# Performance work log

Measured on AMD Instinct MI355X. Metric: run time of the kernel, lower is better.

Reference implementation:

```python
import jax, jax.numpy as jnp
import numpy as np
import math

# dims
B, S, HID = 1, 4096, 2048
NH = 16            # num_attention_heads
Q_LORA = 768
KV_LORA = 512
D_ROPE = 64        # qk_rope_head_dim
D_V = 128          # v_head_dim
TOP_K = 1024       # dsa_top_k
EPS = 1e-6
ROPE_BASE = 1e7
YARN_SCALE = 32.0


def _rms_norm(x, w, eps=EPS):
    xf = x.astype(jnp.float32)
    var = jnp.mean(xf * xf, axis=-1, keepdims=True)
    return (w * (xf * jax.lax.rsqrt(var + eps))).astype(x.dtype)


def _rotate_half(x):
    h = x.shape[-1] // 2
    return jnp.concatenate([-x[..., h:], x[..., :h]], axis=-1)


def _yarn_cos_sin(seq_len):
    # _yarn_find_correction_dims returns (mid, mid) => entire inv_freq is interpolated (divided by scale)
    inv_freq = 1.0 / (ROPE_BASE ** (jnp.arange(0, D_ROPE, 2, dtype=jnp.float32) / D_ROPE))
    inv_freq = inv_freq / YARN_SCALE
    t = jnp.arange(seq_len, dtype=jnp.float32) / YARN_SCALE
    freqs = t[:, None] * inv_freq[None, :]          # [S, D_ROPE/2]
    emb = jnp.concatenate([freqs, freqs], axis=-1)  # [S, D_ROPE]
    mscale2 = (0.1 * math.log(YARN_SCALE) + 1.0) ** 2  # mscale * mscale_all_dim
    return jnp.cos(emb) * mscale2, jnp.sin(emb) * mscale2


def setup_inputs() -> dict:
    key = jax.random.key(0)
    ks = jax.random.split(key, 10)
    std = 0.02
    return {
        'hidden_states': jax.random.normal(ks[0], (B, S, HID), dtype=jnp.float32),
        'position_ids': jnp.broadcast_to(jnp.arange(S), (B, S)),
        'dsa_indices': jnp.sort(jax.random.randint(ks[1], (B, 1, TOP_K), 0, S), axis=-1),
        'wq_a': jax.random.normal(ks[2], (HID, Q_LORA), dtype=jnp.float32) * std,
        'q_a_ln_w': jnp.ones((Q_LORA,), dtype=jnp.float32),
        'wq_b': jax.random.normal(ks[3], (Q_LORA, NH * D_V), dtype=jnp.float32) * std,
        'wq_rope': jax.random.normal(ks[4], (Q_LORA, NH * D_ROPE), dtype=jnp.float32) * std,
        'wkv_a': jax.random.normal(ks[5], (HID, KV_LORA + D_ROPE), dtype=jnp.float32) * std,
        'kv_a_ln_w': jnp.ones((KV_LORA,), dtype=jnp.float32),
        'wkv_b': jax.random.normal(ks[6], (KV_LORA, NH * 2 * D_V), dtype=jnp.float32) * std,
        'wo': jax.random.normal(ks[7], (NH * D_V, HID), dtype=jnp.float32) * std,
    }


def reference(hidden_states, position_ids, dsa_indices, wq_a, q_a_ln_w, wq_b,
              wq_rope, wkv_a, kv_a_ln_w, wkv_b, wo):
    bsz, seq_len, _ = hidden_states.shape

    # low-rank Q path (MLA)
    q_latent = _rms_norm(hidden_states @ wq_a, q_a_ln_w)            # [B,S,Q_LORA]
    q = (q_latent @ wq_b).reshape(bsz, seq_len, NH, D_V)            # [B,S,H,D_V]
    q_rope = (q_latent @ wq_rope).reshape(bsz, seq_len, NH, D_ROPE)

    # low-rank KV path with MQA rope channel
    kv_lr = hidden_states @ wkv_a                                   # [B,S,KV_LORA+D_ROPE]
    kv_latent = _rms_norm(kv_lr[..., :KV_LORA], kv_a_ln_w)
    k_rope = kv_lr[..., KV_LORA:]                                   # [B,S,D_ROPE]
    k_and_v = (kv_latent @ wkv_b).reshape(bsz, seq_len, NH, 2 * D_V)
    k = k_and_v[..., :D_V]
    v = k_and_v[..., D_V:]
    k_rope = jnp.broadcast_to(k_rope[:, :, None, :], (bsz, seq_len, NH, D_ROPE))

    # YaRN rotary embedding
    cos, sin = _yarn_cos_sin(seq_len)                               # [S,D_ROPE]
    cos_p = cos[position_ids][:, :, None, :]                        # [B,S,1,D_ROPE]
    sin_p = sin[position_ids][:, :, None, :]
    q_rope = q_rope * cos_p + _rotate_half(q_rope) * sin_p
    k_rope = k_rope * cos_p + _rotate_half(k_rope) * sin_p

    q_full = jnp.concatenate([q, q_rope], axis=-1)                  # [B,S,H,D_V+D_ROPE]
    k_full = jnp.concatenate([k, k_rope], axis=-1)

    # DSA: gather top-k KV positions per batch (dsa_indices[b,0,:])
    idx = dsa_indices[:, 0, :]                                      # [B,TOP_K]
    k_g = jnp.take_along_axis(k_full, idx[:, :, None, None], axis=1)  # [B,K,H,D]
    v_g = jnp.take_along_axis(v, idx[:, :, None, None], axis=1)       # [B,K,H,D_V]

    scale = 1.0 / math.sqrt(D_V + D_ROPE)
    scores = jnp.einsum('bqhd,bkhd->bhqk', q_full, k_g) * scale     # [B,H,S,K]
    probs = jax.nn.softmax(scores, axis=-1)
    attn = jnp.einsum('bhqk,bkhd->bqhd', probs, v_g)                # [B,S,H,D_V]
    out = attn.reshape(bsz, seq_len, NH * D_V) @ wo                 # [B,S,HID]
    return out
```

## Files before the change

kernel.cpp:

```cpp
#include <hip/hip_runtime.h>
#include <hip/hip_bf16.h>
#include <math.h>

#define S_LEN 4096
#define HIDDEN 2048
#define NH 16
#define QLORA 768
#define KVLORA 512
#define DROPE 64
#define DV 128
#define TOPK 1024
#define DQK 192

typedef __attribute__((ext_vector_type(4))) float f32x4;
typedef __attribute__((ext_vector_type(8))) __bf16 bf16x8;
typedef unsigned short u16;
typedef unsigned int u32;

__device__ __forceinline__ u16 f2bf(float f) {
    union { float f; u32 u; } v; v.f = f;
    u32 r = v.u + 0x7fffu + ((v.u >> 16) & 1u);
    return (u16)(r >> 16);
}

__device__ __forceinline__ void gll16(const u16* g, u16* l) {
    __builtin_amdgcn_global_load_lds((const void*)g, (void*)l, 16, 0, 0);
}

__global__ __launch_bounds__(256) void k_cast(const float* __restrict__ src,
                                              u16* __restrict__ dst, int n4) {
    int i = blockIdx.x * 256 + threadIdx.x;
    if (i >= n4) return;
    float4 v = ((const float4*)src)[i];
    union { u16 h[4]; uint2 u; } o;
    o.h[0] = f2bf(v.x); o.h[1] = f2bf(v.y);
    o.h[2] = f2bf(v.z); o.h[3] = f2bf(v.w);
    ((uint2*)dst)[i] = o.u;
}

__global__ __launch_bounds__(256) void k_yarn(const int* __restrict__ pos_ids,
                                              float* __restrict__ cos_t,
                                              float* __restrict__ sin_t) {
    int idx = blockIdx.x * 256 + threadIdx.x;
    if (idx >= S_LEN * 32) return;
    int s = idx >> 5, i = idx & 31;
    float pos = (float)pos_ids[s];
    float inv = expf(-(float)i * 0.503690489092448f) * (1.0f / 1024.0f);
    float ang = pos * inv;
    const float MS2 = 1.8132604f;
    float sv, cv;
    sincosf(ang, &sv, &cv);
    cos_t[idx] = cv * MS2;
    sin_t[idx] = sv * MS2;
}

__global__ __launch_bounds__(256) void k_transpose(const float* __restrict__ src,
                                                   u16* __restrict__ dst,
                                                   int K, int N) {
    __shared__ u16 t[32][33];
    int n0 = blockIdx.x * 32, k0 = blockIdx.y * 32;
    int tx = threadIdx.x & 31, ty = threadIdx.x >> 5;
    #pragma unroll
    for (int i = 0; i < 32; i += 8)
        t[ty + i][tx] = f2bf(src[(long)(k0 + ty + i) * N + n0 + tx]);
    __syncthreads();
    #pragma unroll
    for (int i = 0; i < 32; i += 8)
        dst[(long)(n0 + ty + i) * K + k0 + tx] = t[tx][ty + i];
}

template <int MODE>
__global__ __launch_bounds__(256) void k_gemm(const u16* __restrict__ A,
                                              const u16* __restrict__ Bt,
                                              void* __restrict__ out0,
                                              void* __restrict__ out1,
                                              const float* __restrict__ cos_t,
                                              const float* __restrict__ sin_t,
                                              int M, int N, int K) {
    __shared__ u16 lA[128 * 32];
    __shared__ u16 lB[128 * 32];
    const int bm = blockIdx.y, bn = blockIdx.x;
    const int tid = threadIdx.x;
    const int lane = tid & 63, wid = tid >> 6;
    const int wr = wid >> 1, wc = wid & 1;
    const int l15 = lane & 15, l4 = lane >> 4;

    f32x4 acc[4][4];
    #pragma unroll
    for (int i = 0; i < 4; ++i)
        #pragma unroll
        for (int j = 0; j < 4; ++j) acc[i][j] = f32x4{0.f, 0.f, 0.f, 0.f};

    const int srow = wid * 32 + (lane >> 2);
    const int scol = (lane & 3) * 8;
    const u16* gA = A + (long)(bm * 128 + srow) * K + scol;
    const u16* gB = Bt + (long)(bn * 128 + srow) * K + scol;
    u16* lA0 = lA + wid * 1024;
    u16* lB0 = lB + wid * 1024;
    const long kstep16 = 16L * K;

    const int nkt = K >> 5;
    for (int kt = 0; kt < nkt; ++kt) {
        const u16* pa = gA + kt * 32;
        const u16* pb = gB + kt * 32;
        gll16(pa, lA0);
        gll16(pa + kstep16, lA0 + 512);
        gll16(pb, lB0);
        gll16(pb + kstep16, lB0 + 512);
        __syncthreads();

        bf16x8 af[4], bfr[4];
        #pragma unroll
        for (int mr = 0; mr < 4; ++mr)
            af[mr] = *(const bf16x8*)(&lA[(wr * 64 + mr * 16 + l15) * 32 + l4 * 8]);
        #pragma unroll
        for (int nc = 0; nc < 4; ++nc)
            bfr[nc] = *(const bf16x8*)(&lB[(wc * 64 + nc * 16 + l15) * 32 + l4 * 8]);
        #pragma unroll
        for (int mr = 0; mr < 4; ++mr)
            #pragma unroll
            for (int nc = 0; nc < 4; ++nc)
                acc[mr][nc] = __builtin_amdgcn_mfma_f32_16x16x32_bf16(
                    af[mr], bfr[nc], acc[mr][nc], 0, 0, 0);
        __syncthreads();
    }

    const int row0 = bm * 128 + wr * 64;
    const int col0 = bn * 128 + wc * 64;
    #pragma unroll
    for (int mr = 0; mr < 4; ++mr) {
        #pragma unroll
        for (int nc = 0; nc < 4; ++nc) {
            #pragma unroll
            for (int jj = 0; jj < 4; ++jj) {
                int row = row0 + mr * 16 + l4 * 4 + jj;
                int col = col0 + nc * 16 + l15;
                float v = acc[mr][nc][jj];
                if (MODE == 0) {
                    if (col < QLORA)
                        ((float*)out0)[(long)row * QLORA + col] = v;
                    else if (col < QLORA + KVLORA + DROPE)
                        ((float*)out1)[(long)row * (KVLORA + DROPE) + (col - QLORA)] = v;
                } else if (MODE == 1) {
                    if (col < NH * DV) {
                        int h = col >> 7, d = col & 127;
                        ((u16*)out0)[((long)h * S_LEN + row) * DQK + d] = f2bf(v);
                    } else {
                        int c2 = col - NH * DV;
                        int h = c2 >> 6, j = c2 & 63, i = j & 31;
                        float c = cos_t[row * 32 + i], sn = sin_t[row * 32 + i];
                        float xp = acc[mr][nc ^ 2][jj];
                        float val = (j < 32) ? v * c - xp * sn : v * c + xp * sn;
                        ((u16*)out0)[((long)h * S_LEN + row) * DQK + DV + j] = f2bf(val);
                    }
                } else if (MODE == 2) {
                    int h = col >> 8, rr = col & 255;
                    if (rr < 128)
                        ((u16*)out0)[((long)h * S_LEN + row) * DV + rr] = f2bf(v);
                    else
                        ((u16*)out1)[((long)h * S_LEN + row) * DV + (rr - 128)] = f2bf(v);
                } else {
                    ((float*)out0)[(long)row * N + col] = v;
                }
            }
        }
    }
}

__global__ __launch_bounds__(256) void k_rms_q(const float* __restrict__ q_lr,
                                               const float* __restrict__ w,
                                               u16* __restrict__ q_latent) {
    int s = blockIdx.x;
    const float* x = q_lr + (long)s * QLORA;
    int t = threadIdx.x;
    float v0 = x[t], v1 = x[t + 256], v2 = x[t + 512];
    float ss = v0 * v0 + v1 * v1 + v2 * v2;
    #pragma unroll
    for (int off = 32; off >= 1; off >>= 1) ss += __shfl_xor(ss, off);
    __shared__ float red[4];
    if ((t & 63) == 0) red[t >> 6] = ss;
    __syncthreads();
    ss = red[0] + red[1] + red[2] + red[3];
    float inv = rsqrtf(ss / (float)QLORA + 1e-6f);
    u16* o = q_latent + (long)s * QLORA;
    o[t]       = f2bf(v0 * inv * w[t]);
    o[t + 256] = f2bf(v1 * inv * w[t + 256]);
    o[t + 512] = f2bf(v2 * inv * w[t + 512]);
}

__global__ __launch_bounds__(256) void k_kv_norm_rope(const float* __restrict__ kv_lr,
                                                      const float* __restrict__ w,
                                                      const float* __restrict__ cos_t,
                                                      const float* __restrict__ sin_t,
                                                      u16* __restrict__ kv_latent,
                                                      u16* __restrict__ krope) {
    int s = blockIdx.x;
    const float* x = kv_lr + (long)s * (KVLORA + DROPE);
    int t = threadIdx.x;
    float v0 = x[t], v1 = x[t + 256];
    float ss = v0 * v0 + v1 * v1;
    #pragma unroll
    for (int off = 32; off >= 1; off >>= 1) ss += __shfl_xor(ss, off);
    __shared__ float red[4];
    if ((t & 63) == 0) red[t >> 6] = ss;
    __syncthreads();
    ss = red[0] + red[1] + red[2] + red[3];
    float inv = rsqrtf(ss / (float)KVLORA + 1e-6f);
    u16* o = kv_latent + (long)s * KVLORA;
    o[t]       = f2bf(v0 * inv * w[t]);
    o[t + 256] = f2bf(v1 * inv * w[t + 256]);
    if (t < DROPE) {
        int i = t & 31;
        float c = cos_t[s * 32 + i], sn = sin_t[s * 32 + i];
        float xr = x[KVLORA + t];
        float xp = x[KVLORA + ((t < 32) ? t + 32 : t - 32)];
        float val = (t < 32) ? xr * c - xp * sn : xr * c + xp * sn;
        krope[(long)s * DROPE + t] = f2bf(val);
    }
}

__global__ void k_gather(const int* __restrict__ idx,
                         const u16* __restrict__ k_buf,
                         const u16* __restrict__ v_buf,
                         const u16* __restrict__ krope,
                         u16* __restrict__ k_g, u16* __restrict__ v_g_t) {
    int j = blockIdx.x, h = blockIdx.y, t = threadIdx.x;
    int src = idx[j];
    const uint4* kb = (const uint4*)(k_buf + ((long)h * S_LEN + src) * DV);
    const uint4* kr = (const uint4*)(krope + (long)src * DROPE);
    uint4* kgp = (uint4*)(k_g + ((long)h * TOPK + j) * DQK);
    if (t < 16)       kgp[t] = kb[t];
    else if (t < 24)  kgp[t] = kr[t - 16];
    u32 vv = *(const u32*)(v_buf + ((long)h * S_LEN + src) * DV + t * 2);
    int kt = j >> 6, jin = j & 63;
    u16* base = v_g_t + ((long)(h * 16 + kt) * 128) * 64 + jin;
    base[(2 * t) * 64]     = (u16)(vv & 0xffff);
    base[(2 * t + 1) * 64] = (u16)(vv >> 16);
}

__global__ __launch_bounds__(256) void k_attn(const u16* __restrict__ qf,
                                              const u16* __restrict__ kg,
                                              const u16* __restrict__ vgt,
                                              u16* __restrict__ attn_out) {
    __shared__ u16 lK[64 * 200];
    __shared__ u16 lVt[128 * 72];
    __shared__ u16 lP[4][16 * 72];
    const int b = blockIdx.x;
    const int h = (b & 7) * 2 + ((b >> 3) & 1);
    const int qt = b >> 4;
    const int tid = threadIdx.x, lane = tid & 63, wid = tid >> 6;
    const int l15 = lane & 15, l4 = lane >> 4;

    bf16x8 qfr[2][6];
    #pragma unroll
    for (int qs = 0; qs < 2; ++qs) {
        const u16* qrow = qf + ((long)h * S_LEN + qt * 128 + wid * 32 + qs * 16 + l15) * DQK + l4 * 8;
        #pragma unroll
        for (int kd = 0; kd < 6; ++kd) qfr[qs][kd] = *(const bf16x8*)(qrow + kd * 32);
    }
    float m[2][4], l[2][4];
    #pragma unroll
    for (int qs = 0; qs < 2; ++qs)
        #pragma unroll
        for (int jj = 0; jj < 4; ++jj) { m[qs][jj] = -1e30f; l[qs][jj] = 0.f; }
    f32x4 acc_o[2][8];
    #pragma unroll
    for (int qs = 0; qs < 2; ++qs)
        #pragma unroll
        for (int nc = 0; nc < 8; ++nc) acc_o[qs][nc] = f32x4{0.f, 0.f, 0.f, 0.f};

    const int krow = tid >> 2, kseg = (tid & 3) * 48;
    u16* lPw = lP[wid];
    const float scale = 0.07216878364870323f;

    for (int kt = 0; kt < TOPK / 64; ++kt) {
        {
            const u16* src = kg + ((long)h * TOPK + kt * 64 + krow) * DQK + kseg;
            u16* dst = &lK[krow * 200 + kseg];
            #pragma unroll
            for (int u = 0; u < 6; ++u)
                *(uint4*)(dst + u * 8) = *(const uint4*)(src + u * 8);
        }
        {
            const u16* src = vgt + ((long)(h * 16 + kt) * 128) * 64 + tid * 32;
            u16* dst = &lVt[(tid >> 1) * 72 + (tid & 1) * 32];
            #pragma unroll
            for (int c = 0; c < 4; ++c)
                *(uint4*)(dst + c * 8) = *(const uint4*)(src + c * 8);
        }
        __syncthreads();

        #pragma unroll
        for (int qs = 0; qs < 2; ++qs) {
            f32x4 sa[4];
            #pragma unroll
            for (int kc = 0; kc < 4; ++kc) {
                sa[kc] = f32x4{0.f, 0.f, 0.f, 0.f};
                #pragma unroll
                for (int kd = 0; kd < 6; ++kd) {
                    bf16x8 kf = *(const bf16x8*)(&lK[(kc * 16 + l15) * 200 + kd * 32 + l4 * 8]);
                    sa[kc] = __builtin_amdgcn_mfma_f32_16x16x32_bf16(qfr[qs][kd], kf, sa[kc], 0, 0, 0);
                }
                sa[kc] *= scale;
            }
            float fac[4], psum[4];
            #pragma unroll
            for (int jj = 0; jj < 4; ++jj) {
                float mx = fmaxf(fmaxf(sa[0][jj], sa[1][jj]), fmaxf(sa[2][jj], sa[3][jj]));
                #pragma unroll
                for (int off = 1; off <= 8; off <<= 1) mx = fmaxf(mx, __shfl_xor(mx, off));
                float mnew = fmaxf(m[qs][jj], mx);
                fac[jj] = __expf(m[qs][jj] - mnew);
                m[qs][jj] = mnew;
                psum[jj] = 0.f;
            }
            #pragma unroll
            for (int kc = 0; kc < 4; ++kc) {
                #pragma unroll
                for (int jj = 0; jj < 4; ++jj) {
                    float p = __expf(sa[kc][jj] - m[qs][jj]);
                    psum[jj] += p;
                    lPw[(l4 * 4 + jj) * 72 + kc * 16 + l15] = f2bf(p);
                }
            }
            #pragma unroll
            for (int jj = 0; jj < 4; ++jj) {
                #pragma unroll
                for (int off = 1; off <= 8; off <<= 1) psum[jj] += __shfl_xor(psum[jj], off);
                l[qs][jj] = l[qs][jj] * fac[jj] + psum[jj];
            }
            #pragma unroll
            for (int nc = 0; nc < 8; ++nc)
                #pragma unroll
                for (int jj = 0; jj < 4; ++jj) acc_o[qs][nc][jj] *= fac[jj];
            #pragma unroll
            for (int kc2 = 0; kc2 < 2; ++kc2) {
                bf16x8 pf = *(const bf16x8*)(&lPw[l15 * 72 + kc2 * 32 + l4 * 8]);
                #pragma unroll
                for (int nc = 0; nc < 8; ++nc) {
                    bf16x8 vf = *(const bf16x8*)(&lVt[(nc * 16 + l15) * 72 + kc2 * 32 + l4 * 8]);
                    acc_o[qs][nc] = __builtin_amdgcn_mfma_f32_16x16x32_bf16(pf, vf, acc_o[qs][nc], 0, 0, 0);
                }
            }
        }
        __syncthreads();
    }
    #pragma unroll
    for (int qs = 0; qs < 2; ++qs) {
        int row = qt * 128 + wid * 32 + qs * 16 + l4 * 4;
        #pragma unroll
        for (int nc = 0; nc < 8; ++nc)
            #pragma unroll
            for (int jj = 0; jj < 4; ++jj) {
                float v = acc_o[qs][nc][jj] / l[qs][jj];
                attn_out[(long)(row + jj) * (NH * DV) + h * DV + nc * 16 + l15] = f2bf(v);
            }
    }
}

extern "C" void kernel_launch(void* const* d_in, const int* in_sizes, int n_in,
                              void* d_out, int out_size, void* d_ws, size_t ws_size,
                              hipStream_t stream) {
    const float* hs      = (const float*)d_in[0];
    const int*   pos     = (const int*)d_in[1];
    const int*   dsa     = (const int*)d_in[2];
    const float* wq_a    = (const float*)d_in[3];
    const float* q_ln    = (const float*)d_in[4];
    const float* wq_b    = (const float*)d_in[5];
    const float* wq_rope = (const float*)d_in[6];
    const float* wkv_a   = (const float*)d_in[7];
    const float* kv_ln   = (const float*)d_in[8];
    const float* wkv_b   = (const float*)d_in[9];
    const float* wo      = (const float*)d_in[10];
    float* out = (float*)d_out;

    char* ws = (char*)d_ws;
    auto alloc = [&](size_t bytes) {
        char* p = ws; ws += (bytes + 255) & ~(size_t)255; return p;
    };
    u16* W1t  = (u16*)alloc(1408L * 2048 * 2);
    u16* W2t  = (u16*)alloc(3072L * 768 * 2);
    u16* W3t  = (u16*)alloc(4096L * 512 * 2);
    u16* W4t  = (u16*)alloc(2048L * 2048 * 2);
    float* q_lr  = (float*)alloc(4096L * 768 * 4);
    float* kv_lr = (float*)alloc(4096L * 576 * 4);
    u16* q_latent   = (u16*)alloc(4096L * 768 * 2);
    u16* kv_latent  = (u16*)alloc(4096L * 512 * 2);
    u16* q_full     = (u16*)alloc(16L * 4096 * 192 * 2);
    u16* k_buf      = (u16*)alloc(16L * 4096 * 128 * 2);
    u16* v_buf      = (u16*)alloc(16L * 4096 * 128 * 2);
    float* cos_t    = (float*)alloc(4096L * 32 * 4);
    float* sin_t    = (float*)alloc(4096L * 32 * 4);
    char* late = alloc(16L * 4096 * 2 * 2);
    u16* hs_bf = (u16*)late;
    u16* k_g   = (u16*)late;
    u16* v_g_t = k_g + 16L * 1024 * 192;
    u16* krope = v_g_t + 16L * 1024 * 128;
    u16* attn_o = (u16*)q_lr;

    k_yarn<<<dim3(512), dim3(256), 0, stream>>>(pos, cos_t, sin_t);
    k_cast<<<dim3(8192), dim3(256), 0, stream>>>(hs, hs_bf, 4096 * 2048 / 4);

    k_transpose<<<dim3(768 / 32, 2048 / 32), 256, 0, stream>>>(wq_a, W1t, 2048, 768);
    k_transpose<<<dim3(576 / 32, 2048 / 32), 256, 0, stream>>>(wkv_a, W1t + 768L * 2048, 2048, 576);
    k_transpose<<<dim3(2048 / 32, 768 / 32), 256, 0, stream>>>(wq_b, W2t, 768, 2048);
    k_transpose<<<dim3(1024 / 32, 768 / 32), 256, 0, stream>>>(wq_rope, W2t + 2048L * 768, 768, 1024);
    k_transpose<<<dim3(4096 / 32, 512 / 32), 256, 0, stream>>>(wkv_b, W3t, 512, 4096);
    k_transpose<<<dim3(2048 / 32, 2048 / 32), 256, 0, stream>>>(wo, W4t, 2048, 2048);

    k_gemm<0><<<dim3(11, 32), 256, 0, stream>>>(hs_bf, W1t, q_lr, kv_lr, nullptr, nullptr, 4096, 1408, 2048);
    k_rms_q<<<4096, 256, 0, stream>>>(q_lr, q_ln, q_latent);
    k_kv_norm_rope<<<4096, 256, 0, stream>>>(kv_lr, kv_ln, cos_t, sin_t, kv_latent, krope);
    k_gemm<1><<<dim3(24, 32), 256, 0, stream>>>(q_latent, W2t, q_full, nullptr, cos_t, sin_t, 4096, 3072, 768);
    k_gemm<2><<<dim3(32, 32), 256, 0, stream>>>(kv_latent, W3t, k_buf, v_buf, nullptr, nullptr, 4096, 4096, 512);
    k_gather<<<dim3(1024, 16), 64, 0, stream>>>(dsa, k_buf, v_buf, krope, k_g, v_g_t);
    k_attn<<<dim3(512), 256, 0, stream>>>(q_full, k_g, v_g_t, attn_o);
    k_gemm<3><<<dim3(16, 32), 256, 0, stream>>>(attn_o, W4t, out, nullptr, nullptr, nullptr, 4096, 2048, 2048);
}
```

Baseline: 502.4 us.

## Load K and V fragments directly from global memory, drop LDS staging and barriers

The attention kernel no longer stages K and V tiles into shared memory with block-wide barriers. Each wave now loads its MFMA fragments straight from global memory and reuses each K/V fragment across both 16-row query sub-tiles. A per-subtile P buffer lets the PV MFMAs for both sub-tiles be interleaved. This removes the LDS round trip and the __syncthreads stalls and raises occupancy through lower LDS use. In exchange, all 4 waves re-read the same K/V from global/L2 with strided 16-byte accesses.

After: 554.7 us. +10.4%, slower.

```diff
diff --git a/kernel.cpp b/kernel.cpp
--- a/kernel.cpp
+++ b/kernel.cpp
@@ -242,9 +242,7 @@
                                               const u16* __restrict__ kg,
                                               const u16* __restrict__ vgt,
                                               u16* __restrict__ attn_out) {
-    __shared__ u16 lK[64 * 200];
-    __shared__ u16 lVt[128 * 72];
-    __shared__ u16 lP[4][16 * 72];
+    __shared__ u16 lP[4][2][16 * 72];
     const int b = blockIdx.x;
     const int h = (b & 7) * 2 + ((b >> 3) & 1);
     const int qt = b >> 4;
@@ -269,44 +267,33 @@
         #pragma unroll
         for (int nc = 0; nc < 8; ++nc) acc_o[qs][nc] = f32x4{0.f, 0.f, 0.f, 0.f};
 
-    const int krow = tid >> 2, kseg = (tid & 3) * 48;
-    u16* lPw = lP[wid];
     const float scale = 0.07216878364870323f;
 
     for (int kt = 0; kt < TOPK / 64; ++kt) {
-        {
-            const u16* src = kg + ((long)h * TOPK + kt * 64 + krow) * DQK + kseg;
-            u16* dst = &lK[krow * 200 + kseg];
-            #pragma unroll
-            for (int u = 0; u < 6; ++u)
-                *(uint4*)(dst + u * 8) = *(const uint4*)(src + u * 8);
+        f32x4 sa[2][4];
+        #pragma unroll
+        for (int kc = 0; kc < 4; ++kc) {
+            const u16* kbase = kg + ((long)h * TOPK + kt * 64 + kc * 16 + l15) * DQK + l4 * 8;
+            bf16x8 kf[6];
+            #pragma unroll
+            for (int kd = 0; kd < 6; ++kd) kf[kd] = *(const bf16x8*)(kbase + kd * 32);
+            sa[0][kc] = f32x4{0.f, 0.f, 0.f, 0.f};
+            sa[1][kc] = f32x4{0.f, 0.f, 0.f, 0.f};
+            #pragma unroll
+            for (int kd = 0; kd < 6; ++kd) {
+                sa[0][kc] = __builtin_amdgcn_mfma_f32_16x16x32_bf16(qfr[0][kd], kf[kd], sa[0][kc], 0, 0, 0);
+                sa[1][kc] = __builtin_amdgcn_mfma_f32_16x16x32_bf16(qfr[1][kd], kf[kd], sa[1][kc], 0, 0, 0);
+            }
+            sa[0][kc] *= scale;
+            sa[1][kc] *= scale;
         }
-        {
-            const u16* src = vgt + ((long)(h * 16 + kt) * 128) * 64 + tid * 32;
-            u16* dst = &lVt[(tid >> 1) * 72 + (tid & 1) * 32];
-            #pragma unroll
-            for (int c = 0; c < 4; ++c)
-                *(uint4*)(dst + c * 8) = *(const uint4*)(src + c * 8);
-        }
-        __syncthreads();
-
         #pragma unroll
         for (int qs = 0; qs < 2; ++qs) {
-            f32x4 sa[4];
-            #pragma unroll
-            for (int kc = 0; kc < 4; ++kc) {
-                sa[kc] = f32x4{0.f, 0.f, 0.f, 0.f};
-                #pragma unroll
-                for (int kd = 0; kd < 6; ++kd) {
-                    bf16x8 kf = *(const bf16x8*)(&lK[(kc * 16 + l15) * 200 + kd * 32 + l4 * 8]);
-                    sa[kc] = __builtin_amdgcn_mfma_f32_16x16x32_bf16(qfr[qs][kd], kf, sa[kc], 0, 0, 0);
-                }
-                sa[kc] *= scale;
-            }
             float fac[4], psum[4];
             #pragma unroll
             for (int jj = 0; jj < 4; ++jj) {
-                float mx = fmaxf(fmaxf(sa[0][jj], sa[1][jj]), fmaxf(sa[2][jj], sa[3][jj]));
+                float mx = fmaxf(fmaxf(sa[qs][0][jj], sa[qs][1][jj]),
+                                 fmaxf(sa[qs][2][jj], sa[qs][3][jj]));
                 #pragma unroll
                 for (int off = 1; off <= 8; off <<= 1) mx = fmaxf(mx, __shfl_xor(mx, off));
                 float mnew = fmaxf(m[qs][jj], mx);
@@ -318,9 +305,9 @@
             for (int kc = 0; kc < 4; ++kc) {
                 #pragma unroll
                 for (int jj = 0; jj < 4; ++jj) {
-                    float p = __expf(sa[kc][jj] - m[qs][jj]);
+                    float p = __expf(sa[qs][kc][jj] - m[qs][jj]);
                     psum[jj] += p;
-                    lPw[(l4 * 4 + jj) * 72 + kc * 16 + l15] = f2bf(p);
+                    lP[wid][qs][(l4 * 4 + jj) * 72 + kc * 16 + l15] = f2bf(p);
                 }
             }
             #pragma unroll
@@ -333,17 +320,19 @@
             for (int nc = 0; nc < 8; ++nc)
                 #pragma unroll
                 for (int jj = 0; jj < 4; ++jj) acc_o[qs][nc][jj] *= fac[jj];
-            #pragma unroll
-            for (int kc2 = 0; kc2 < 2; ++kc2) {
-                bf16x8 pf = *(const bf16x8*)(&lPw[l15 * 72 + kc2 * 32 + l4 * 8]);
-                #pragma unroll
-                for (int nc = 0; nc < 8; ++nc) {
-                    bf16x8 vf = *(const bf16x8*)(&lVt[(nc * 16 + l15) * 72 + kc2 * 32 + l4 * 8]);
-                    acc_o[qs][nc] = __builtin_amdgcn_mfma_f32_16x16x32_bf16(pf, vf, acc_o[qs][nc], 0, 0, 0);
-                }
-            }
         }
-        __syncthreads();
+        #pragma unroll
+        for (int kc2 = 0; kc2 < 2; ++kc2) {
+            bf16x8 pf0 = *(const bf16x8*)(&lP[wid][0][l15 * 72 + kc2 * 32 + l4 * 8]);
+            bf16x8 pf1 = *(const bf16x8*)(&lP[wid][1][l15 * 72 + kc2 * 32 + l4 * 8]);
+            #pragma unroll
+            for (int nc = 0; nc < 8; ++nc) {
+                const u16* vbase = vgt + ((long)(h * 16 + kt) * 128 + nc * 16 + l15) * 64 + kc2 * 32 + l4 * 8;
+                bf16x8 vf = *(const bf16x8*)(vbase);
+                acc_o[0][nc] = __builtin_amdgcn_mfma_f32_16x16x32_bf16(pf0, vf, acc_o[0][nc], 0, 0, 0);
+                acc_o[1][nc] = __builtin_amdgcn_mfma_f32_16x16x32_bf16(pf1, vf, acc_o[1][nc], 0, 0, 0);
+            }
+        }
     }
     #pragma unroll
     for (int qs = 0; qs < 2; ++qs) {
```

## Restructure attention kernel with swizzled K tiles, async LDS prefetch, direct V reads

Applied to the files above, without the earlier changes.

The gather kernel now writes K tiles in an XOR-swizzled layout, so the attention kernel can fill LDS with direct global-to-LDS loads (gll16) and prefetch the next tile while the PV product runs. V is no longer staged in LDS; each wave reads it straight from global memory. Each block now covers 64 queries instead of 128, doubling the grid, and the kernel adds launch bounds for higher occupancy plus s_setprio around the MFMA sections. In exchange, V is re-read from global/L2 by every wave, and the diff relies on a gll16 helper defined in the unseen part of the file.

Result: no change. 493.9 us (-1.7%).

```diff
diff --git a/kernel.cpp b/kernel.cpp
--- a/kernel.cpp
+++ b/kernel.cpp
@@ -223,27 +223,28 @@
                          const u16* __restrict__ k_buf,
                          const u16* __restrict__ v_buf,
                          const u16* __restrict__ krope,
-                         u16* __restrict__ k_g, u16* __restrict__ v_g_t) {
+                         u16* __restrict__ kgs, u16* __restrict__ vg) {
     int j = blockIdx.x, h = blockIdx.y, t = threadIdx.x;
     int src = idx[j];
-    const uint4* kb = (const uint4*)(k_buf + ((long)h * S_LEN + src) * DV);
-    const uint4* kr = (const uint4*)(krope + (long)src * DROPE);
-    uint4* kgp = (uint4*)(k_g + ((long)h * TOPK + j) * DQK);
-    if (t < 16)       kgp[t] = kb[t];
-    else if (t < 24)  kgp[t] = kr[t - 16];
+    int kt = j >> 6, jin = j & 63;
+    if (t < 24) {
+        uint4 val;
+        if (t < 16) val = ((const uint4*)(k_buf + ((long)h * S_LEN + src) * DV))[t];
+        else        val = ((const uint4*)(krope + (long)src * DROPE))[t - 16];
+        int su = t ^ (jin & 7);
+        ((uint4*)(kgs + (long)(h * 16 + kt) * 12288 + jin * 192))[su] = val;
+    }
     u32 vv = *(const u32*)(v_buf + ((long)h * S_LEN + src) * DV + t * 2);
-    int kt = j >> 6, jin = j & 63;
-    u16* base = v_g_t + ((long)(h * 16 + kt) * 128) * 64 + jin;
+    u16* base = vg + ((long)(h * 16 + kt) * 128) * 64 + jin;
     base[(2 * t) * 64]     = (u16)(vv & 0xffff);
     base[(2 * t + 1) * 64] = (u16)(vv >> 16);
 }
 
-__global__ __launch_bounds__(256) void k_attn(const u16* __restrict__ qf,
-                                              const u16* __restrict__ kg,
-                                              const u16* __restrict__ vgt,
-                                              u16* __restrict__ attn_out) {
-    __shared__ u16 lK[64 * 200];
-    __shared__ u16 lVt[128 * 72];
+__global__ __launch_bounds__(256, 4) void k_attn(const u16* __restrict__ qf,
+                                                 const u16* __restrict__ kgs,
+                                                 const u16* __restrict__ vg,
+                                                 u16* __restrict__ attn_out) {
+    __shared__ u16 lK[64 * 192];
     __shared__ u16 lP[4][16 * 72];
     const int b = blockIdx.x;
     const int h = (b & 7) * 2 + ((b >> 3) & 1);
@@ -251,111 +252,105 @@
     const int tid = threadIdx.x, lane = tid & 63, wid = tid >> 6;
     const int l15 = lane & 15, l4 = lane >> 4;
 
-    bf16x8 qfr[2][6];
-    #pragma unroll
-    for (int qs = 0; qs < 2; ++qs) {
-        const u16* qrow = qf + ((long)h * S_LEN + qt * 128 + wid * 32 + qs * 16 + l15) * DQK + l4 * 8;
-        #pragma unroll
-        for (int kd = 0; kd < 6; ++kd) qfr[qs][kd] = *(const bf16x8*)(qrow + kd * 32);
-    }
-    float m[2][4], l[2][4];
-    #pragma unroll
-    for (int qs = 0; qs < 2; ++qs)
-        #pragma unroll
-        for (int jj = 0; jj < 4; ++jj) { m[qs][jj] = -1e30f; l[qs][jj] = 0.f; }
-    f32x4 acc_o[2][8];
-    #pragma unroll
-    for (int qs = 0; qs < 2; ++qs)
-        #pragma unroll
-        for (int nc = 0; nc < 8; ++nc) acc_o[qs][nc] = f32x4{0.f, 0.f, 0.f, 0.f};
-
-    const int krow = tid >> 2, kseg = (tid & 3) * 48;
+    bf16x8 qfr[6];
+    {
+        const u16* qrow = qf + ((long)h * S_LEN + qt * 64 + wid * 16 + l15) * DQK + l4 * 8;
+        #pragma unroll
+        for (int kd = 0; kd < 6; ++kd) qfr[kd] = *(const bf16x8*)(qrow + kd * 32);
+    }
+    float m[4] = {-1e30f, -1e30f, -1e30f, -1e30f};
+    float l[4] = {0.f, 0.f, 0.f, 0.f};
+    f32x4 acc[8];
+    #pragma unroll
+    for (int nc = 0; nc < 8; ++nc) acc[nc] = f32x4{0.f, 0.f, 0.f, 0.f};
+
+    const float scale = 0.07216878364870323f;
+    const u16* ktile = kgs + (long)h * 16 * 12288;
     u16* lPw = lP[wid];
-    const float scale = 0.07216878364870323f;
+
+    {
+        const u16* src = ktile + wid * 512 + lane * 8;
+        u16* dst = lK + wid * 512;
+        #pragma unroll
+        for (int i = 0; i < 6; ++i) gll16(src + i * 2048, dst + i * 2048);
+    }
 
     for (int kt = 0; kt < TOPK / 64; ++kt) {
-        {
-            const u16* src = kg + ((long)h * TOPK + kt * 64 + krow) * DQK + kseg;
-            u16* dst = &lK[krow * 200 + kseg];
-            #pragma unroll
-            for (int u = 0; u < 6; ++u)
-                *(uint4*)(dst + u * 8) = *(const uint4*)(src + u * 8);
-        }
-        {
-            const u16* src = vgt + ((long)(h * 16 + kt) * 128) * 64 + tid * 32;
-            u16* dst = &lVt[(tid >> 1) * 72 + (tid & 1) * 32];
-            #pragma unroll
-            for (int c = 0; c < 4; ++c)
-                *(uint4*)(dst + c * 8) = *(const uint4*)(src + c * 8);
-        }
         __syncthreads();
-
-        #pragma unroll
-        for (int qs = 0; qs < 2; ++qs) {
-            f32x4 sa[4];
-            #pragma unroll
-            for (int kc = 0; kc < 4; ++kc) {
-                sa[kc] = f32x4{0.f, 0.f, 0.f, 0.f};
-                #pragma unroll
-                for (int kd = 0; kd < 6; ++kd) {
-                    bf16x8 kf = *(const bf16x8*)(&lK[(kc * 16 + l15) * 200 + kd * 32 + l4 * 8]);
-                    sa[kc] = __builtin_amdgcn_mfma_f32_16x16x32_bf16(qfr[qs][kd], kf, sa[kc], 0, 0, 0);
-                }
-                sa[kc] *= scale;
+        f32x4 sa[4];
+        __builtin_amdgcn_s_setprio(1);
+        #pragma unroll
+        for (int kc = 0; kc < 4; ++kc) {
+            sa[kc] = f32x4{0.f, 0.f, 0.f, 0.f};
+            int r = kc * 16 + l15;
+            #pragma unroll
+            for (int kd = 0; kd < 6; ++kd) {
+                int cu = kd * 4 + l4;
+                bf16x8 kf = *(const bf16x8*)(&lK[r * 192 + ((cu ^ (r & 7)) * 8)]);
+                sa[kc] = __builtin_amdgcn_mfma_f32_16x16x32_bf16(qfr[kd], kf, sa[kc], 0, 0, 0);
             }
-            float fac[4], psum[4];
+            sa[kc] *= scale;
+        }
+        __builtin_amdgcn_s_setprio(0);
+        float fac[4], psum[4];
+        #pragma unroll
+        for (int jj = 0; jj < 4; ++jj) {
+            float mx = fmaxf(fmaxf(sa[0][jj], sa[1][jj]), fmaxf(sa[2][jj], sa[3][jj]));
+            #pragma unroll
+            for (int off = 1; off <= 8; off <<= 1) mx = fmaxf(mx, __shfl_xor(mx, off));
+            float mnew = fmaxf(m[jj], mx);
+            fac[jj] = __expf(m[jj] - mnew);
+            m[jj] = mnew;
+            psum[jj] = 0.f;
+        }
+        #pragma unroll
+        for (int kc = 0; kc < 4; ++kc) {
             #pragma unroll
             for (int jj = 0; jj < 4; ++jj) {
-                float mx = fmaxf(fmaxf(sa[0][jj], sa[1][jj]), fmaxf(sa[2][jj], sa[3][jj]));
-                #pragma unroll
-                for (int off = 1; off <= 8; off <<= 1) mx = fmaxf(mx, __shfl_xor(mx, off));
-                float mnew = fmaxf(m[qs][jj], mx);
-                fac[jj] = __expf(m[qs][jj] - mnew);
-                m[qs][jj] = mnew;
-                psum[jj] = 0.f;
+                float p = __expf(sa[kc][jj] - m[jj]);
+                psum[jj] += p;
+                lPw[(l4 * 4 + jj) * 72 + kc * 16 + l15] = f2bf(p);
             }
-            #pragma unroll
-            for (int kc = 0; kc < 4; ++kc) {
-                #pragma unroll
-                for (int jj = 0; jj < 4; ++jj) {
-                    float p = __expf(sa[kc][jj] - m[qs][jj]);
-                    psum[jj] += p;
-                    lPw[(l4 * 4 + jj) * 72 + kc * 16 + l15] = f2bf(p);
-                }
+        }
+        #pragma unroll
+        for (int jj = 0; jj < 4; ++jj) {
+            #pragma unroll
+            for (int off = 1; off <= 8; off <<= 1) psum[jj] += __shfl_xor(psum[jj], off);
+            l[jj] = l[jj] * fac[jj] + psum[jj];
+        }
+        #pragma unroll
+        for (int nc = 0; nc < 8; ++nc)
+            #pragma unroll
+            for (int jj = 0; jj < 4; ++jj) acc[nc][jj] *= fac[jj];
+
+        __syncthreads();
+        if (kt < TOPK / 64 - 1) {
+            const u16* src = ktile + (kt + 1) * 12288 + wid * 512 + lane * 8;
+            u16* dst = lK + wid * 512;
+            #pragma unroll
+            for (int i = 0; i < 6; ++i) gll16(src + i * 2048, dst + i * 2048);
+        }
+        __builtin_amdgcn_s_setprio(1);
+        #pragma unroll
+        for (int kc2 = 0; kc2 < 2; ++kc2) {
+            bf16x8 pf = *(const bf16x8*)(&lPw[l15 * 72 + kc2 * 32 + l4 * 8]);
+            #pragma unroll
+            for (int nc = 0; nc < 8; ++nc) {
+                const u16* vbase = vg + ((long)(h * 16 + kt) * 128 + nc * 16 + l15) * 64 + kc2 * 32 + l4 * 8;
+                bf16x8 vf = *(const bf16x8*)(vbase);
+                acc[nc] = __builtin_amdgcn_mfma_f32_16x16x32_bf16(pf, vf, acc[nc], 0, 0, 0);
             }
-            #pragma unroll
-            for (int jj = 0; jj < 4; ++jj) {
-                #pragma unroll
-                for (int off = 1; off <= 8; off <<= 1) psum[jj] += __shfl_xor(psum[jj], off);
-                l[qs][jj] = l[qs][jj] * fac[jj] + psum[jj];
-            }
-            #pragma unroll
-            for (int nc = 0; nc < 8; ++nc)
-                #pragma unroll
-                for (int jj = 0; jj < 4; ++jj) acc_o[qs][nc][jj] *= fac[jj];
-            #pragma unroll
-            for (int kc2 = 0; kc2 < 2; ++kc2) {
-                bf16x8 pf = *(const bf16x8*)(&lPw[l15 * 72 + kc2 * 32 + l4 * 8]);
-                #pragma unroll
-                for (int nc = 0; nc < 8; ++nc) {
-                    bf16x8 vf = *(const bf16x8*)(&lVt[(nc * 16 + l15) * 72 + kc2 * 32 + l4 * 8]);
-                    acc_o[qs][nc] = __builtin_amdgcn_mfma_f32_16x16x32_bf16(pf, vf, acc_o[qs][nc], 0, 0, 0);
-                }
-            }
-        }
-        __syncthreads();
-    }
-    #pragma unroll
-    for (int qs = 0; qs < 2; ++qs) {
-        int row = qt * 128 + wid * 32 + qs * 16 + l4 * 4;
-        #pragma unroll
-        for (int nc = 0; nc < 8; ++nc)
-            #pragma unroll
-            for (int jj = 0; jj < 4; ++jj) {
-                float v = acc_o[qs][nc][jj] / l[qs][jj];
-                attn_out[(long)(row + jj) * (NH * DV) + h * DV + nc * 16 + l15] = f2bf(v);
-            }
-    }
+        }
+        __builtin_amdgcn_s_setprio(0);
+    }
+    int row = qt * 64 + wid * 16 + l4 * 4;
+    #pragma unroll
+    for (int nc = 0; nc < 8; ++nc)
+        #pragma unroll
+        for (int jj = 0; jj < 4; ++jj) {
+            float v = acc[nc][jj] / l[jj];
+            attn_out[(long)(row + jj) * (NH * DV) + h * DV + nc * 16 + l15] = f2bf(v);
+        }
 }
 
 extern "C" void kernel_launch(void* const* d_in, const int* in_sizes, int n_in,
@@ -393,9 +388,9 @@
     float* sin_t    = (float*)alloc(4096L * 32 * 4);
     char* late = alloc(16L * 4096 * 2 * 2);
     u16* hs_bf = (u16*)late;
-    u16* k_g   = (u16*)late;
-    u16* v_g_t = k_g + 16L * 1024 * 192;
-    u16* krope = v_g_t + 16L * 1024 * 128;
+    u16* kgs   = (u16*)late;
+    u16* vg    = kgs + 16L * 16 * 12288;
+    u16* krope = vg + 16L * 1024 * 128;
     u16* attn_o = (u16*)q_lr;
 
     k_yarn<<<dim3(512), dim3(256), 0, stream>>>(pos, cos_t, sin_t);
@@ -413,7 +408,7 @@
     k_kv_norm_rope<<<4096, 256, 0, stream>>>(kv_lr, kv_ln, cos_t, sin_t, kv_latent, krope);
     k_gemm<1><<<dim3(24, 32), 256, 0, stream>>>(q_latent, W2t, q_full, nullptr, cos_t, sin_t, 4096, 3072, 768);
     k_gemm<2><<<dim3(32, 32), 256, 0, stream>>>(kv_latent, W3t, k_buf, v_buf, nullptr, nullptr, 4096, 4096, 512);
-    k_gather<<<dim3(1024, 16), 64, 0, stream>>>(dsa, k_buf, v_buf, krope, k_g, v_g_t);
-    k_attn<<<dim3(512), 256, 0, stream>>>(q_full, k_g, v_g_t, attn_o);
+    k_gather<<<dim3(1024, 16), 64, 0, stream>>>(dsa, k_buf, v_buf, krope, kgs, vg);
+    k_attn<<<dim3(1024), 256, 0, stream>>>(q_full, kgs, vg, attn_o);
     k_gemm<3><<<dim3(16, 32), 256, 0, stream>>>(attn_o, W4t, out, nullptr, nullptr, nullptr, 4096, 2048, 2048);
 }
```
